# Kernel tuning notes

Measured on AMD Instinct MI355X. Metric: run time of the kernel, lower is better.

## Reference

```python
import jax, jax.numpy as jnp
import numpy as np

R, C, B, E, H = 16, 256, 12, 768, 12  # rows, cols, batch(==heads, see notes), embed, heads
D = E // H
NUM_BUCKETS, MAX_DISTANCE = 32, 50000


def _relative_position_bucket(distances):
    # T5-style log-spaced buckets, matching the torch code (trunc toward zero).
    n = jnp.abs(distances)
    max_exact = NUM_BUCKETS // 2
    is_small = n < max_exact
    nf = jnp.maximum(n.astype(jnp.float32), 1.0)  # guard log(0); masked by is_small
    val_large = max_exact + (
        jnp.log(nf / max_exact) / np.log(MAX_DISTANCE / max_exact) * (NUM_BUCKETS - max_exact - 1)
    ).astype(jnp.int32)
    val_large = jnp.minimum(val_large, NUM_BUCKETS - 1)
    return jnp.where(is_small, n.astype(jnp.int32), val_large)


def setup_inputs() -> dict:
    key = jax.random.key(0)
    ks = jax.random.split(key, 11)
    s = 1.0 / np.sqrt(E)
    x = jax.random.normal(ks[0], (R, C, B, E), jnp.float32)
    distances = jax.random.randint(ks[1], (B, C, C), 0, MAX_DISTANCE, jnp.int32)
    Wq = jax.random.normal(ks[2], (E, E), jnp.float32) * s
    bq = jnp.zeros((E,), jnp.float32)
    Wk = jax.random.normal(ks[3], (E, E), jnp.float32) * s
    bk = jnp.zeros((E,), jnp.float32)
    Wv = jax.random.normal(ks[4], (E, E), jnp.float32) * s
    bv = jnp.zeros((E,), jnp.float32)
    Wo = jax.random.normal(ks[5], (E, E), jnp.float32) * s
    bo = jnp.zeros((E,), jnp.float32)
    rel_bias = jax.random.normal(ks[6], (NUM_BUCKETS, H), jnp.float32) * 0.02
    return dict(x=x, distances=distances, Wq=Wq, bq=bq, Wk=Wk, bk=bk,
                Wv=Wv, bv=bv, Wo=Wo, bo=bo, rel_bias=rel_bias)


def reference(x, distances, Wq, bq, Wk, bk, Wv, bv, Wo, bo, rel_bias):
    scaling = (D ** -0.5) / np.sqrt(R)  # align_scaling: head_dim^-0.5 / sqrt(num_rows)
    q = (x @ Wq.T + bq).reshape(R, C, B, H, D) * scaling
    k = (x @ Wk.T + bk).reshape(R, C, B, H, D)
    # row-aggregated scores: sum over rows r -> (h, n, i, j)
    attn = jnp.einsum('rinhd,rjnhd->hnij', q, k)
    # relative position bias: (n, i, j) -> buckets -> (n, i, j, h) -> (n, h, i, j)
    buckets = _relative_position_bucket(distances)
    bias = jnp.transpose(rel_bias[buckets], (0, 3, 1, 2))
    # NOTE: source adds (n,h,i,j) bias onto (h,n,i,j) scores positionally; valid since B == H.
    attn = attn + bias
    probs = jax.nn.softmax(attn, axis=-1)  # (h, n, i, j)
    v = (x @ Wv.T + bv).reshape(R, C, B, H, D)
    ctx = jnp.einsum('hnij,rjnhd->rinhd', probs, v).reshape(R, C, B, E)
    out = ctx @ Wo.T + bo
    return out, probs
```

## Files before the change

### kernel.cpp

```cpp
#include <hip/hip_runtime.h>
#include <stdint.h>
#include <math.h>

#define R_ 16
#define C_ 256
#define B_ 12
#define E_ 768
#define H_ 12
#define D_ 64
#define TOK (R_*C_*B_)
#define HALF_TOK 24576

#define QK_HALF 37748736
#define VT_BASE 37748736
#define VT_QUARTER 9437184
#define CTXQ_ELEMS 9437184

typedef __bf16 bf16x8 __attribute__((ext_vector_type(8)));
typedef float floatx4 __attribute__((ext_vector_type(4)));

__device__ __forceinline__ unsigned short f2bf(float f) {
    union { unsigned int i; float f; } v; v.f = f;
    unsigned int i = v.i;
    return (unsigned short)((i + 0x7fffu + ((i >> 16) & 1u)) >> 16);
}
__device__ __forceinline__ bf16x8 cvt8(floatx4 lo, floatx4 hi) {
    bf16x8 r;
    r[0] = (__bf16)lo[0]; r[1] = (__bf16)lo[1]; r[2] = (__bf16)lo[2]; r[3] = (__bf16)lo[3];
    r[4] = (__bf16)hi[0]; r[5] = (__bf16)hi[1]; r[6] = (__bf16)hi[2]; r[7] = (__bf16)hi[3];
    return r;
}
__device__ __forceinline__ void gload16(const unsigned short* g, unsigned short* l) {
    __builtin_amdgcn_global_load_lds(
        (const __attribute__((address_space(1))) unsigned int*)g,
        (__attribute__((address_space(3))) unsigned int*)l, 16, 0, 0);
}

template<int MODE>
__global__ __launch_bounds__(256)
void gemm_bt(const void* __restrict__ Ap,
             const void* __restrict__ Btp,
             const float* __restrict__ bias,
             void* __restrict__ Cout,
             int nBase)
{
    __shared__ __align__(16) unsigned short As[128 * 32];
    __shared__ __align__(16) unsigned short Bs[128 * 32];

    constexpr bool AGL = (MODE != 2);
    constexpr int K = (MODE == 2) ? 256 : 768;
    constexpr int kIters = K >> 5;
    constexpr int GX = (MODE==0) ? 12 : (MODE==2) ? 2 : (MODE==3) ? 6 : 6;
    constexpr int GY = (MODE==0) ? 192 : (MODE==2) ? 2 : (MODE==3) ? 384 : 96;
    constexpr int GZ = (MODE==2) ? 144 : 1;

    const int tid  = threadIdx.x;
    const int wave = tid >> 6, lane = tid & 63;
    const int quad = lane >> 4, l15 = lane & 15;
    const int wr = wave >> 1, wc = wave & 1;

    const int lin = ((int)blockIdx.z * GY + (int)blockIdx.y) * GX + (int)blockIdx.x;
    const int tt  = (lin & 7) * ((GX * GY * GZ) >> 3) + (lin >> 3);
    const int bx  = tt % GX;
    const int rem = tt / GX;
    const int by  = rem % GY, bz = rem / GY;
    const int row0 = by * 128, col0 = bx * 128;

    int hIdx = 0, nIdx = 0;
    if (MODE == 2) { hIdx = bz % 12; nIdx = bz / 12; }

    const int rA0 = tid >> 2;
    const int ck  = tid & 3;
    const int sw  = (tid >> 3) & 3;
    const int kko = ((ck ^ sw) << 3);

    const unsigned short* Bt = (const unsigned short*)Btp;
    const unsigned short *gB0, *gB1;
    if (MODE == 2) {
        const size_t vq = VT_BASE + (size_t)nBase * VT_QUARTER
                          + ((size_t)(nIdx * 12 + hIdx) * 256) * 256;
        gB0 = Bt + vq + (size_t)(col0 + rA0) * 256 + kko;
        gB1 = Bt + vq + (size_t)(col0 + rA0 + 64) * 256 + kko;
    } else {
        gB0 = Bt + (size_t)(col0 + rA0) * 768 + kko;
        gB1 = Bt + (size_t)(col0 + rA0 + 64) * 768 + kko;
    }

    const unsigned short* gA0u = nullptr; const unsigned short* gA1u = nullptr;
    const float* gA0f = nullptr; const float* gA1f = nullptr;
    if (AGL) {
        gA0u = (const unsigned short*)Ap + (size_t)(row0 + rA0) * 768 + kko;
        gA1u = (const unsigned short*)Ap + (size_t)(row0 + rA0 + 64) * 768 + kko;
    } else {
        gA0f = (const float*)Ap + ((size_t)(hIdx * 12 + nIdx)) * 65536
               + (size_t)(row0 + rA0) * 256 + kko;
        gA1f = (const float*)Ap + ((size_t)(hIdx * 12 + nIdx)) * 65536
               + (size_t)(row0 + rA0 + 64) * 256 + kko;
    }

    unsigned short* lA0 = As + wave * 512;
    unsigned short* lA1 = As + 2048 + wave * 512;
    unsigned short* lB0 = Bs + wave * 512;
    unsigned short* lB1 = Bs + 2048 + wave * 512;

    const floatx4 zero = {0.f, 0.f, 0.f, 0.f};
    floatx4 acc[4][4];
#pragma unroll
    for (int i = 0; i < 4; ++i)
#pragma unroll
        for (int j = 0; j < 4; ++j) acc[i][j] = zero;

    const int chO = ((quad ^ ((l15 >> 1) & 3)) << 3);

    floatx4 u0l = zero, u0h = zero, u1l = zero, u1h = zero;
    floatx4 p0l = zero, p0h = zero, p1l = zero, p1h = zero;
    if (!AGL) {
        u0l = *(const floatx4*)(gA0f);     u0h = *(const floatx4*)(gA0f + 4);
        u1l = *(const floatx4*)(gA1f);     u1h = *(const floatx4*)(gA1f + 4);
    }

#define GSTEP(KT, UL0, UH0, UL1, UH1, PL0, PH0, PL1, PH1)                         \
    {                                                                              \
        __syncthreads();                                \
        gload16(gB0 + (KT) * 32, lB0);                                             \
        gload16(gB1 + (KT) * 32, lB1);                                             \
        if (AGL) {                                                                 \
            gload16(gA0u + (KT) * 32, lA0);                                        \
            gload16(gA1u + (KT) * 32, lA1);                                        \
        } else {                                                                   \
            *(bf16x8*)(As + tid * 8)        = cvt8(UL0, UH0);                      \
            *(bf16x8*)(As + 2048 + tid * 8) = cvt8(UL1, UH1);                      \
        }                                                                          \
        __syncthreads();                                      \
        if (!AGL && ((KT) + 1 < kIters)) {             \
            PL0 = *(const floatx4*)(gA0f + ((KT) + 1) * 32);                       \
            PH0 = *(const floatx4*)(gA0f + ((KT) + 1) * 32 + 4);                   \
            PL1 = *(const floatx4*)(gA1f + ((KT) + 1) * 32);                       \
            PH1 = *(const floatx4*)(gA1f + ((KT) + 1) * 32 + 4);                   \
        }                                                                          \
        bf16x8 af[4], bfr[4];                                                      \
        _Pragma("unroll")                                                          \
        for (int t = 0; t < 4; ++t) {                                              \
            af[t]  = *(const bf16x8*)(As + (wr * 64 + t * 16 + l15) * 32 + chO);   \
            bfr[t] = *(const bf16x8*)(Bs + (wc * 64 + t * 16 + l15) * 32 + chO);   \
        }                                                                          \
        _Pragma("unroll")                                                          \
        for (int tm = 0; tm < 4; ++tm)                                             \
            _Pragma("unroll")                                                      \
            for (int tn = 0; tn < 4; ++tn)                                         \
                acc[tm][tn] = __builtin_amdgcn_mfma_f32_16x16x32_bf16(             \
                    af[tm], bfr[tn], acc[tm][tn], 0, 0, 0);                        \
    }

    for (int kt = 0; kt < kIters; kt += 2) {
        GSTEP(kt,     u0l, u0h, u1l, u1h, p0l, p0h, p1l, p1h);
        GSTEP(kt + 1, p0l, p0h, p1l, p1h, u0l, u0h, u1l, u1h);
    }
#undef GSTEP

#pragma unroll
    for (int tm = 0; tm < 4; ++tm) {
        const int rbase = row0 + wr * 64 + tm * 16 + quad * 4;
#pragma unroll
        for (int tn = 0; tn < 4; ++tn) {
            const int cc = col0 + wc * 64 + tn * 16 + l15;
#pragma unroll
            for (int rr = 0; rr < 4; ++rr) {
                float vv = acc[tm][tn][rr];
                const int rowg = rbase + rr;
                if (MODE == 0) {
                    const int tg = nBase * HALF_TOK + rowg;
                    const int m = tg / 12, n = tg - m * 12;
                    const int r = m >> 8, i = m & 255;
                    const int sel = cc >= 768 ? 1 : 0;
                    const int ccl = cc - sel * 768;
                    const int h = ccl >> 6, d = ccl & 63;
                    ((unsigned short*)Cout)[(size_t)sel * QK_HALF
                        + ((size_t)(n * 12 + h) * 256 + i) * 1024 + r * 64 + d]
                        = f2bf(vv + bias[cc]);
                } else if (MODE == 2) {
                    ((unsigned short*)Cout)[((((size_t)(cc >> 6)) * 256 + rowg) * 12
                        + nIdx) * 768 + hIdx * 64 + (cc & 63)] = f2bf(vv);
                } else if (MODE == 3) {
                    const int m = rowg / 12, n = rowg - m * 12;
                    const int r = m >> 8, j = m & 255;
                    const int h = cc >> 6, d = cc & 63;
                    ((unsigned short*)Cout)[VT_BASE + (size_t)(r >> 2) * VT_QUARTER
                        + ((size_t)(n * 12 + h) * 256 + (r & 3) * 64 + d) * 256 + j]
                        = f2bf(vv + bias[cc]);
                } else {
                    ((float*)Cout)[((size_t)(nBase * 12288 + rowg)) * 768 + cc]
                        = vv + bias[cc];
                }
            }
        }
    }
}

__global__ __launch_bounds__(512)
void scores_sm(const unsigned short* __restrict__ q,
               const unsigned short* __restrict__ k,
               const int* __restrict__ buckets,
               const float* __restrict__ rb,
               float* __restrict__ probs)
{
    __shared__ __align__(16) unsigned short As[128 * 32];
    __shared__ __align__(16) unsigned short Bs[256 * 32];

    const int tid  = threadIdx.x;
    const int w    = tid >> 6, lane = tid & 63;
    const int quad = lane >> 4, l15 = lane & 15;

    const int lin = (int)blockIdx.z * 2 + (int)blockIdx.y;
    const int tt  = (lin & 7) * 36 + (lin >> 3);
    const int by  = tt % 2, bz = tt / 2;
    const int row0 = by * 128;
    const int h = bz % 12, n = bz / 12;

    const int rA0 = tid >> 2;
    const int ck  = tid & 3;
    const int sw  = (tid >> 3) & 3;
    const int kko = ((ck ^ sw) << 3);

    const unsigned short* gA  = q + ((size_t)bz * 256 + row0 + rA0) * 1024 + kko;
    const unsigned short* gB0 = k + ((size_t)bz * 256 + rA0) * 1024 + kko;
    const unsigned short* gB1 = k + ((size_t)bz * 256 + rA0 + 128) * 1024 + kko;

    unsigned short* lA  = As + w * 512;
    unsigned short* lB0 = Bs + w * 512;
    unsigned short* lB1 = Bs + 4096 + w * 512;

    const floatx4 zero = {0.f, 0.f, 0.f, 0.f};
    floatx4 acc[16];
#pragma unroll
    for (int t = 0; t < 16; ++t) acc[t] = zero;

    const int chO = ((quad ^ ((l15 >> 1) & 3)) << 3);

    for (int kt = 0; kt < 32; ++kt) {
        __syncthreads();
        gload16(gA  + kt * 32, lA);
        gload16(gB0 + kt * 32, lB0);
        gload16(gB1 + kt * 32, lB1);
        __syncthreads();
        const bf16x8 af = *(const bf16x8*)(As + (w * 16 + l15) * 32 + chO);
#pragma unroll
        for (int tn = 0; tn < 16; ++tn) {
            const bf16x8 bfr = *(const bf16x8*)(Bs + (tn * 16 + l15) * 32 + chO);
            acc[tn] = __builtin_amdgcn_mfma_f32_16x16x32_bf16(af, bfr, acc[tn], 0, 0, 0);
        }
    }

    const int i0 = row0 + w * 16 + quad * 4;
    float mx[4] = {-3.4e38f, -3.4e38f, -3.4e38f, -3.4e38f};
#pragma unroll
    for (int tn = 0; tn < 16; ++tn) {
        const int j = tn * 16 + l15;
#pragma unroll
        for (int rr = 0; rr < 4; ++rr) {
            const int bkt = buckets[((size_t)h * 256 + i0 + rr) * 256 + j];
            const float s = acc[tn][rr] * 0.03125f + rb[bkt * 12 + n];
            acc[tn][rr] = s;
            mx[rr] = fmaxf(mx[rr], s);
        }
    }
#pragma unroll
    for (int rr = 0; rr < 4; ++rr)
#pragma unroll
        for (int off = 1; off < 16; off <<= 1)
            mx[rr] = fmaxf(mx[rr], __shfl_xor(mx[rr], off, 64));
    float sm[4] = {0.f, 0.f, 0.f, 0.f};
#pragma unroll
    for (int tn = 0; tn < 16; ++tn)
#pragma unroll
        for (int rr = 0; rr < 4; ++rr) {
            const float e = expf(acc[tn][rr] - mx[rr]);
            acc[tn][rr] = e;
            sm[rr] += e;
        }
#pragma unroll
    for (int rr = 0; rr < 4; ++rr)
#pragma unroll
        for (int off = 1; off < 16; off <<= 1)
            sm[rr] += __shfl_xor(sm[rr], off, 64);
    float inv[4];
#pragma unroll
    for (int rr = 0; rr < 4; ++rr) inv[rr] = 1.f / sm[rr];

    float* prow = probs + ((size_t)(h * 12 + n)) * 65536;
#pragma unroll
    for (int tn = 0; tn < 16; ++tn) {
        const int j = tn * 16 + l15;
#pragma unroll
        for (int rr = 0; rr < 4; ++rr)
            prow[(size_t)(i0 + rr) * 256 + j] = acc[tn][rr] * inv[rr];
    }
}

__global__ __launch_bounds__(256)
void cvt_bulk(const float* __restrict__ src, unsigned short* __restrict__ dst, int n)
{
    const int i = (blockIdx.x * 256 + threadIdx.x) * 8;
    if (i >= n) return;
    floatx4 a = ((const floatx4*)(src + i))[0];
    floatx4 b = ((const floatx4*)(src + i))[1];
    *(bf16x8*)(dst + i) = cvt8(a, b);
}

__global__ __launch_bounds__(256)
void prep(const int* __restrict__ dist, int* __restrict__ buckets,
          const float* __restrict__ Wq, const float* __restrict__ Wk,
          const float* __restrict__ Wv, const float* __restrict__ Wo,
          const float* __restrict__ bq, const float* __restrict__ bk,
          unsigned short* __restrict__ wqk, unsigned short* __restrict__ wvb,
          unsigned short* __restrict__ wob, float* __restrict__ bqk)
{
    if (blockIdx.x < 3072) {
        const int idx = blockIdx.x * 256 + threadIdx.x;
        if (idx >= B_ * C_ * C_) return;
        const int dv = dist[idx];
        const int n = dv < 0 ? -dv : dv;
        int bkt;
        if (n < 16) {
            bkt = n;
        } else {
            const float lg = logf((float)n * 0.0625f);
            const float t  = (lg / 8.047189562170502f) * 15.0f;
            bkt = 16 + (int)t;
            if (bkt > 31) bkt = 31;
        }
        buckets[idx] = bkt;
        return;
    }
    const int gid = (blockIdx.x - 3072) * 256 + threadIdx.x;
    const int W8 = 73728;
    if (gid < 4 * W8) {
        const int sec = gid / W8, off = (gid - sec * W8) * 8;
        const float* src = (sec == 0) ? Wq : (sec == 1) ? Wk : (sec == 2) ? Wv : Wo;
        unsigned short* dst = (sec == 0) ? wqk : (sec == 1) ? (wqk + 589824)
                              : (sec == 2) ? wvb : wob;
        floatx4 a = ((const floatx4*)(src + off))[0];
        floatx4 b = ((const floatx4*)(src + off))[1];
        *(bf16x8*)(dst + off) = cvt8(a, b);
    } else {
        const int b = gid - 4 * W8;
        if (b < 1536) bqk[b] = (b < 768) ? bq[b] : bk[b - 768];
    }
}

extern "C" void kernel_launch(void* const* d_in, const int* in_sizes, int n_in,
                              void* d_out, int out_size, void* d_ws, size_t ws_size,
                              hipStream_t stream)
{
    const float* x    = (const float*)d_in[0];
    const int*   dist = (const int*)d_in[1];
    const float* Wq   = (const float*)d_in[2];
    const float* bq   = (const float*)d_in[3];
    const float* Wk   = (const float*)d_in[4];
    const float* bk   = (const float*)d_in[5];
    const float* Wv   = (const float*)d_in[6];
    const float* bv   = (const float*)d_in[7];
    const float* Wo   = (const float*)d_in[8];
    const float* bo   = (const float*)d_in[9];
    const float* rb   = (const float*)d_in[10];

    float* outp  = (float*)d_out;
    float* probs = (float*)d_out + (size_t)TOK * E_;

    unsigned short* dob  = (unsigned short*)d_out;
    unsigned short* qs   = dob;
    unsigned short* ks   = dob + QK_HALF;
    unsigned short* x_bf = (unsigned short*)probs;

    char* ws = (char*)d_ws;
    unsigned short* wo_bf  = (unsigned short*)(ws);
    unsigned short* wv_bf  = (unsigned short*)(ws + 1179648);
    float*          bqk    = (float*)(ws + 2359296);
    unsigned short* ctx_q  = (unsigned short*)(ws + 2365440);
    int*            buckets= (int*)(ws + 21239808);
    unsigned short* wqk_bf = (unsigned short*)(ws + 24385536);

    dim3 blk(256);

    prep<<<dim3(4230), blk, 0, stream>>>(dist, buckets, Wq, Wk, Wv, Wo, bq, bk,
                                         wqk_bf, wv_bf, wo_bf, bqk);

    for (int half = 0; half < 2; ++half) {
        cvt_bulk<<<dim3(9216), blk, 0, stream>>>(
            x + (size_t)half * HALF_TOK * 768, x_bf, HALF_TOK * 768);
        gemm_bt<0><<<dim3(12, 192), blk, 0, stream>>>(x_bf, wqk_bf, bqk, qs, half);
    }

    scores_sm<<<dim3(1, 2, 144), dim3(512), 0, stream>>>(qs, ks, buckets, rb, probs);

    cvt_bulk<<<dim3(18432), blk, 0, stream>>>(x, dob, TOK * E_);
    gemm_bt<3><<<dim3(6, 384), blk, 0, stream>>>(dob, wv_bf, bv, dob, 0);
    for (int q = 0; q < 4; ++q) {
        gemm_bt<2><<<dim3(2, 2, 144), blk, 0, stream>>>(probs, dob, nullptr, ctx_q, q);
        gemm_bt<4><<<dim3(6, 96), blk, 0, stream>>>(ctx_q, wo_bf, bo, outp, q);
    }
}
```

Before: 941.7 us.

## Compute V projection transposed so output stores are contiguous along j

The V projection is swapped from x·Wvᵀ to Wv·xᵀ per batch n. The x conversion now reorders tokens into n-major layout, so each GEMM tile's columns map to consecutive j positions of the transposed V buffer. The old version scattered each output element with a 256-element stride. The change adds index arithmetic to the conversion kernel, and the bias is now indexed by row instead of column.

```diff
diff --git a/kernel.cpp b/kernel.cpp
--- a/kernel.cpp
+++ b/kernel.cpp
@@ -14,7 +14,6 @@
 #define QK_HALF 37748736
 #define VT_BASE 37748736
 #define VT_QUARTER 9437184
-#define CTXQ_ELEMS 9437184
 
 typedef __bf16 bf16x8 __attribute__((ext_vector_type(8)));
 typedef float floatx4 __attribute__((ext_vector_type(4)));
@@ -50,9 +49,9 @@
     constexpr bool AGL = (MODE != 2);
     constexpr int K = (MODE == 2) ? 256 : 768;
     constexpr int kIters = K >> 5;
-    constexpr int GX = (MODE==0) ? 12 : (MODE==2) ? 2 : (MODE==3) ? 6 : 6;
-    constexpr int GY = (MODE==0) ? 192 : (MODE==2) ? 2 : (MODE==3) ? 384 : 96;
-    constexpr int GZ = (MODE==2) ? 144 : 1;
+    constexpr int GX = (MODE==0) ? 12 : (MODE==2) ? 2 : (MODE==3) ? 32 : 6;
+    constexpr int GY = (MODE==0) ? 192 : (MODE==2) ? 2 : (MODE==3) ? 6 : 96;
+    constexpr int GZ = (MODE==2) ? 144 : (MODE==3) ? 12 : 1;
 
     const int tid  = threadIdx.x;
     const int wave = tid >> 6, lane = tid & 63;
@@ -68,6 +67,7 @@
 
     int hIdx = 0, nIdx = 0;
     if (MODE == 2) { hIdx = bz % 12; nIdx = bz / 12; }
+    if (MODE == 3) { nIdx = bz; }
 
     const int rA0 = tid >> 2;
     const int ck  = tid & 3;
@@ -81,6 +81,9 @@
                           + ((size_t)(nIdx * 12 + hIdx) * 256) * 256;
         gB0 = Bt + vq + (size_t)(col0 + rA0) * 256 + kko;
         gB1 = Bt + vq + (size_t)(col0 + rA0 + 64) * 256 + kko;
+    } else if (MODE == 3) {
+        gB0 = Bt + ((size_t)nIdx * 4096 + col0 + rA0) * 768 + kko;
+        gB1 = Bt + ((size_t)nIdx * 4096 + col0 + rA0 + 64) * 768 + kko;
     } else {
         gB0 = Bt + (size_t)(col0 + rA0) * 768 + kko;
         gB1 = Bt + (size_t)(col0 + rA0 + 64) * 768 + kko;
@@ -182,12 +185,11 @@
                     ((unsigned short*)Cout)[((((size_t)(cc >> 6)) * 256 + rowg) * 12
                         + nIdx) * 768 + hIdx * 64 + (cc & 63)] = f2bf(vv);
                 } else if (MODE == 3) {
-                    const int m = rowg / 12, n = rowg - m * 12;
-                    const int r = m >> 8, j = m & 255;
-                    const int h = cc >> 6, d = cc & 63;
+                    const int h = rowg >> 6, d = rowg & 63;
+                    const int r = cc >> 8, j = cc & 255;
                     ((unsigned short*)Cout)[VT_BASE + (size_t)(r >> 2) * VT_QUARTER
-                        + ((size_t)(n * 12 + h) * 256 + (r & 3) * 64 + d) * 256 + j]
-                        = f2bf(vv + bias[cc]);
+                        + ((size_t)(nIdx * 12 + h) * 256 + (r & 3) * 64 + d) * 256 + j]
+                        = f2bf(vv + bias[rowg]);
                 } else {
                     ((float*)Cout)[((size_t)(nBase * 12288 + rowg)) * 768 + cc]
                         = vv + bias[cc];
@@ -305,6 +307,18 @@
     floatx4 a = ((const floatx4*)(src + i))[0];
     floatx4 b = ((const floatx4*)(src + i))[1];
     *(bf16x8*)(dst + i) = cvt8(a, b);
+}
+
+__global__ __launch_bounds__(256)
+void cvt_xn(const float* __restrict__ src, unsigned short* __restrict__ dst)
+{
+    const size_t flat = ((size_t)blockIdx.x * 256 + threadIdx.x) * 8;
+    const int tok = (int)(flat / 768);
+    const int e   = (int)(flat - (size_t)tok * 768);
+    const int n = tok % 12, m = tok / 12;
+    floatx4 a = ((const floatx4*)(src + flat))[0];
+    floatx4 b = ((const floatx4*)(src + flat))[1];
+    *(bf16x8*)(dst + ((size_t)(n * 4096 + m)) * 768 + e) = cvt8(a, b);
 }
 
 __global__ __launch_bounds__(256)
@@ -393,8 +407,8 @@
 
     scores_sm<<<dim3(1, 2, 144), dim3(512), 0, stream>>>(qs, ks, buckets, rb, probs);
 
-    cvt_bulk<<<dim3(18432), blk, 0, stream>>>(x, dob, TOK * E_);
-    gemm_bt<3><<<dim3(6, 384), blk, 0, stream>>>(dob, wv_bf, bv, dob, 0);
+    cvt_xn<<<dim3(18432), blk, 0, stream>>>(x, dob);
+    gemm_bt<3><<<dim3(32, 6, 12), blk, 0, stream>>>(wv_bf, dob, bv, dob, 0);
     for (int q = 0; q < 4; ++q) {
         gemm_bt<2><<<dim3(2, 2, 144), blk, 0, stream>>>(probs, dob, nullptr, ctx_q, q);
         gemm_bt<4><<<dim3(6, 96), blk, 0, stream>>>(ctx_q, wo_bf, bo, outp, q);
```

New measurement: 862.0 us. 8.5% less time.
